# Performance work log

Measured on AMD Instinct MI355X. Metric: run time of the kernel, lower is better.

## Reference

```python
import jax, jax.numpy as jnp
import numpy as np

_DIR_INLIER = 0.9          # _HOUGHVOTING_DIRECTION_INLIER
_NUM_INLIER = 500          # _HOUGHVOTING_NUM_INLIER
_LABEL_THRESH = 500        # _LABEL2MASK_THRESHOL
NUM_CLASSES = 10
BS, H, W = 1, 240, 320


def setup_inputs() -> dict:
    key = jax.random.key(0)
    k_lab, k_cx, k_cy, k_nx, k_ny, k_nd = jax.random.split(key, 6)
    label = jax.random.randint(k_lab, (BS, H, W), 0, NUM_CLASSES + 1).astype(jnp.int32)
    xs = jnp.arange(W, dtype=jnp.float32)
    ys = jnp.arange(H, dtype=jnp.float32)
    xv, yv = jnp.meshgrid(xs, ys)  # [H, W] each
    # per-class ground-truth centers well inside the image so voting converges
    cxs = jax.random.uniform(k_cx, (NUM_CLASSES,), minval=40.0, maxval=W - 40.0)
    cys = jax.random.uniform(k_cy, (NUM_CLASSES,), minval=40.0, maxval=H - 40.0)
    dx = cxs[:, None, None] - xv[None]  # [C, H, W]
    dy = cys[:, None, None] - yv[None]
    nrm = jnp.sqrt(dx * dx + dy * dy) + 1e-6
    dirx = dx / nrm + 0.01 * jax.random.normal(k_nx, (NUM_CLASSES, H, W))
    diry = dy / nrm + 0.01 * jax.random.normal(k_ny, (NUM_CLASSES, H, W))
    depth = (1.0 + 0.3 * jnp.arange(NUM_CLASSES, dtype=jnp.float32))[:, None, None] \
        + 0.01 * jax.random.normal(k_nd, (NUM_CLASSES, H, W))
    cmap = jnp.stack([dirx, diry, depth], axis=1).reshape(3 * NUM_CLASSES, H, W)
    centermap = jnp.broadcast_to(cmap[None], (BS, 3 * NUM_CLASSES, H, W)).astype(jnp.float32)
    return {"label": label, "centermap": centermap}


def hough_voting(label, centermap, num_classes):
    bs, H_, W_ = label.shape
    xs = jnp.arange(W_, dtype=jnp.float32)
    ys = jnp.arange(H_, dtype=jnp.float32)
    xv, yv = jnp.meshgrid(xs, ys)            # [H, W]
    xsi = jnp.arange(W_, dtype=jnp.int32)
    all_centers, all_depths = [], []
    for b in range(bs):
        lab = label[b]
        row_c, row_d = [], []
        for cls in range(1, num_classes + 1):
            cmask = lab == cls                                    # [H, W]
            enough = cmask.sum() >= _LABEL_THRESH
            c3 = centermap[b, (cls - 1) * 3:(cls - 1) * 3 + 3]    # [3, H, W]
            slope = c3[1] / c3[0]                                  # dy/dx per pixel
            # every masked pixel votes along its line at every column x
            y_idx = jnp.round(yv[:, :, None] + slope[:, :, None] * (xs[None, None, :] - xv[:, :, None])).astype(jnp.int32)  # [H, W, W]
            valid = (y_idx >= 0) & (y_idx < H_) & cmask[:, :, None]
            bins = jnp.clip(y_idx, 0, H_ - 1) * W_ + xsi[None, None, :]
            hist = jnp.zeros(H_ * W_, jnp.float32).at[bins.ravel()].add(valid.ravel().astype(jnp.float32))
            cbin = jnp.argmax(hist)
            inlier_num = hist[cbin]
            cx = (cbin % W_).astype(jnp.float32)
            cy = (cbin // W_).astype(jnp.float32)
            # depth: mean of depth channel over direction-consistent class pixels
            disx = xv - cx
            disy = yv - cy
            dnrm = jnp.sqrt(disx * disx + disy * disy)
            dot = jnp.abs((disx / dnrm) * c3[0] + (disy / dnrm) * c3[1])  # nan at center -> compares False, as torch
            imask = (dot >= _DIR_INLIER) & cmask
            cnt = imask.sum().astype(jnp.float32)
            dsum = jnp.sum(jnp.where(imask, c3[2], 0.0))
            dmean = jnp.where(cnt > 0, dsum / jnp.maximum(cnt, 1.0), jnp.nan)
            trig = enough & (inlier_num > _NUM_INLIER)
            row_c.append(jnp.where(trig, jnp.stack([cx, cy]), jnp.zeros(2, jnp.float32)))
            row_d.append(jnp.where(trig, dmean, 0.0))
        all_centers.append(jnp.stack(row_c))
        all_depths.append(jnp.stack(row_d))
    return jnp.stack(all_centers), jnp.stack(all_depths)


def reference(label, centermap):
    return hough_voting(label, centermap, NUM_CLASSES)
```

## Files before the change

### kernel.cpp

```cpp
#include <hip/hip_runtime.h>
#include <stdint.h>

#define H 240
#define W 320
#define NPIX (H * W)
#define NCLS 10
#define COLS 4
#define VTHR 512
#define BIN_BITS 20
#define BIN_MASK 0xFFFFFu
#define POIS32 0xAAAAAAAAu


__global__ __launch_bounds__(256) void k_compact(const int* __restrict__ label,
                                                 const float* __restrict__ cm,
                                                 uint32_t* __restrict__ cls_cnt,
                                                 uint2* __restrict__ list) {
    __shared__ uint32_t lcnt[NCLS];
    __shared__ uint32_t lbase[NCLS];
    int p = blockIdx.x * 256 + threadIdx.x;
    if (threadIdx.x < NCLS) lcnt[threadIdx.x] = 0;
    __syncthreads();

    int l = label[p];
    bool match = (l >= 1 && l <= NCLS);
    int cls = l - 1;
    uint32_t li = 0;
    if (match) li = atomicAdd(&lcnt[cls], 1u);
    __syncthreads();

    if (threadIdx.x < NCLS) {
        uint32_t c = lcnt[threadIdx.x];
        lbase[threadIdx.x] = c ? (atomicAdd(&cls_cnt[threadIdx.x], c) - POIS32) : 0u;
    }
    __syncthreads();

    if (match) {
        float dirx = cm[(cls * 3 + 0) * NPIX + p];
        float diry = cm[(cls * 3 + 1) * NPIX + p];
        float slope = diry / dirx;
        int y = p / W, x = p - y * W;
        uint2 e;
        e.x = (uint32_t)(x | (y << 16));
        e.y = __float_as_uint(slope);
        list[cls * NPIX + lbase[cls] + li] = e;
    }
}

__global__ __launch_bounds__(VTHR) void k_vote(const uint32_t* __restrict__ cls_cnt,
                                               const uint2* __restrict__ list,
                                               unsigned long long* __restrict__ best) {
    int cls = blockIdx.y;
    int x0 = blockIdx.x * COLS;
    __shared__ uint32_t hist[COLS][H];
    __shared__ unsigned long long wred[VTHR / 64];
    for (int i = threadIdx.x; i < COLS * H; i += VTHR) ((uint32_t*)hist)[i] = 0;
    __syncthreads();

    int n = (int)(cls_cnt[cls] - POIS32);
    const uint2* lst = list + cls * NPIX;
    for (int i0 = 0; i0 < n; i0 += VTHR) {
        int i = i0 + (int)threadIdx.x;
        bool inb = (i < n);
        uint2 e;
        e.x = 0u; e.y = 0u;
        if (inb) e = lst[i];
        float slope = __uint_as_float(e.y);
        float xf = (float)(e.x & 0xFFFFu);
        float yf = (float)(e.x >> 16);
#pragma unroll
        for (int c = 0; c < COLS; ++c) {
            float dx = (float)(x0 + c) - xf;
            float r = rintf(yf + slope * dx);
            bool valid = inb && (r >= 0.0f) && (r <= (float)(H - 1));
            if (valid) atomicAdd(&hist[c][(int)r], 1u);
        }
    }
    __syncthreads();

    unsigned long long k = 0;
    for (int i = threadIdx.x; i < COLS * H; i += VTHR) {
        int c = i / H, y = i - c * H;
        uint32_t v = hist[c][y];
        uint32_t bin = (uint32_t)(y * W + x0 + c);
        unsigned long long key =
            ((unsigned long long)v << BIN_BITS) | (unsigned long long)(BIN_MASK - bin);
        if (key > k) k = key;
    }
#pragma unroll
    for (int off = 32; off > 0; off >>= 1) {
        unsigned long long o = __shfl_down(k, off);
        if (o > k) k = o;
    }
    if ((threadIdx.x & 63u) == 0u) wred[threadIdx.x >> 6] = k;
    __syncthreads();
    if (threadIdx.x == 0) {
        unsigned long long kk = wred[0];
#pragma unroll
        for (int w = 1; w < VTHR / 64; ++w) if (wred[w] > kk) kk = wred[w];
        atomicMax((long long*)&best[cls], (long long)kk);
    }
}

__global__ __launch_bounds__(256) void k_inlier_final(
    const int* __restrict__ label, const float* __restrict__ cm,
    const uint32_t* __restrict__ cls_cnt,
    const unsigned long long* __restrict__ best,
    uint32_t* __restrict__ icnt, float* __restrict__ dsum,
    uint32_t* __restrict__ done, float* __restrict__ out) {
    __shared__ float scx[NCLS], scy[NCLS];
    __shared__ uint32_t scnt[NCLS];
    __shared__ float ssum[NCLS];
    __shared__ int slast;
    int tid = threadIdx.x;
    if (tid < NCLS) {
        unsigned long long key = best[tid];
        uint32_t bin = BIN_MASK - (uint32_t)(key & BIN_MASK);
        scx[tid] = (float)(bin % W);
        scy[tid] = (float)(bin / W);
        scnt[tid] = 0u;
        ssum[tid] = 0.0f;
    }
    __syncthreads();

    int p = blockIdx.x * 256 + tid;
    int l = label[p];
    if (l >= 1 && l <= NCLS) {
        int cls = l - 1;
        int y = p / W, x = p - y * W;
        float disx = (float)x - scx[cls];
        float disy = (float)y - scy[cls];
        float dn = sqrtf(disx * disx + disy * disy);
        if (dn > 0.0f) {
            float c0 = cm[(cls * 3 + 0) * NPIX + p];
            float c1 = cm[(cls * 3 + 1) * NPIX + p];
            float dot = fabsf((disx / dn) * c0 + (disy / dn) * c1);
            if (dot >= 0.9f) {
                atomicAdd(&scnt[cls], 1u);
                atomicAdd(&ssum[cls], cm[(cls * 3 + 2) * NPIX + p]);
            }
        }
    }
    __syncthreads();

    if (tid < NCLS) {
        if (scnt[tid]) atomicAdd(&icnt[tid], scnt[tid]);
        if (ssum[tid] != 0.0f) atomicAdd(&dsum[tid], ssum[tid]);
    }
    if (tid == 0) {
        __threadfence();
        uint32_t d = atomicAdd(done, 1u);
        slast = (d == POIS32 + (uint32_t)(gridDim.x - 1)) ? 1 : 0;
    }
    __syncthreads();

    if (slast && tid < NCLS) {
        uint32_t tc = atomicAdd(&icnt[tid], 0u) - POIS32;
        float td = atomicAdd(&dsum[tid], 0.0f);
        unsigned long long key = best[tid];
        uint32_t hv = (uint32_t)(key >> BIN_BITS);
        bool trig = ((cls_cnt[tid] - POIS32) >= 500u) && (hv > 500u);
        float c = (float)tc;
        float dm = (c > 0.0f) ? (td / fmaxf(c, 1.0f)) : __builtin_nanf("");
        out[tid * 2 + 0] = trig ? scx[tid] : 0.0f;
        out[tid * 2 + 1] = trig ? scy[tid] : 0.0f;
        out[2 * NCLS + tid] = trig ? dm : 0.0f;
    }
}

extern "C" void kernel_launch(void* const* d_in, const int* in_sizes, int n_in,
                              void* d_out, int out_size, void* d_ws, size_t ws_size,
                              hipStream_t stream) {
    const int* label = (const int*)d_in[0];
    const float* cm = (const float*)d_in[1];
    float* out = (float*)d_out;
    char* ws = (char*)d_ws;

    uint32_t* cls_cnt = (uint32_t*)(ws + 0);
    unsigned long long* best = (unsigned long long*)(ws + 64);
    uint32_t* icnt = (uint32_t*)(ws + 192);
    float* dsum = (float*)(ws + 256);
    uint32_t* done = (uint32_t*)(ws + 320);
    uint2* list = (uint2*)(ws + 512);

    k_compact<<<NPIX / 256, 256, 0, stream>>>(label, cm, cls_cnt, list);
    k_vote<<<dim3(W / COLS, NCLS), VTHR, 0, stream>>>(cls_cnt, list, best);
    k_inlier_final<<<NPIX / 256, 256, 0, stream>>>(label, cm, cls_cnt, best,
                                                   icnt, dsum, done, out);
}
```

Measured before the change: 98.35 us.

## Fuse inlier/depth pass into vote kernel via last-block-per-class epilogue

Removes the separate inlier/final kernel. The last vote block to finish for each class, detected with a per-class atomic done counter, reads the best bin and iterates the compacted class pixel list to count direction inliers and sum depth, then writes that class's outputs. This drops a kernel launch and a full-image label scan. In exchange the inlier work for each class is serialized into one block at the tail of voting, with gathered centermap reads.

```diff
diff --git a/kernel.cpp b/kernel.cpp
--- a/kernel.cpp
+++ b/kernel.cpp
@@ -49,18 +49,26 @@
 
 __global__ __launch_bounds__(VTHR) void k_vote(const uint32_t* __restrict__ cls_cnt,
                                                const uint2* __restrict__ list,
-                                               unsigned long long* __restrict__ best) {
+                                               const float* __restrict__ cm,
+                                               unsigned long long* __restrict__ best,
+                                               uint32_t* __restrict__ done_cls,
+                                               float* __restrict__ out) {
     int cls = blockIdx.y;
     int x0 = blockIdx.x * COLS;
     __shared__ uint32_t hist[COLS][H];
     __shared__ unsigned long long wred[VTHR / 64];
-    for (int i = threadIdx.x; i < COLS * H; i += VTHR) ((uint32_t*)hist)[i] = 0;
+    __shared__ int slastS;
+    __shared__ float scx, scy;
+    __shared__ uint32_t shv, scnt;
+    __shared__ float ssum;
+    int tid = threadIdx.x;
+    for (int i = tid; i < COLS * H; i += VTHR) ((uint32_t*)hist)[i] = 0;
     __syncthreads();
 
     int n = (int)(cls_cnt[cls] - POIS32);
     const uint2* lst = list + cls * NPIX;
     for (int i0 = 0; i0 < n; i0 += VTHR) {
-        int i = i0 + (int)threadIdx.x;
+        int i = i0 + tid;
         bool inb = (i < n);
         uint2 e;
         e.x = 0u; e.y = 0u;
@@ -79,7 +87,7 @@
     __syncthreads();
 
     unsigned long long k = 0;
-    for (int i = threadIdx.x; i < COLS * H; i += VTHR) {
+    for (int i = tid; i < COLS * H; i += VTHR) {
         int c = i / H, y = i - c * H;
         uint32_t v = hist[c][y];
         uint32_t bin = (uint32_t)(y * W + x0 + c);
@@ -92,79 +100,58 @@
         unsigned long long o = __shfl_down(k, off);
         if (o > k) k = o;
     }
-    if ((threadIdx.x & 63u) == 0u) wred[threadIdx.x >> 6] = k;
+    if ((tid & 63) == 0) wred[tid >> 6] = k;
     __syncthreads();
-    if (threadIdx.x == 0) {
+    if (tid == 0) {
         unsigned long long kk = wred[0];
 #pragma unroll
         for (int w = 1; w < VTHR / 64; ++w) if (wred[w] > kk) kk = wred[w];
         atomicMax((long long*)&best[cls], (long long)kk);
+        __threadfence();
+        uint32_t d = atomicAdd(&done_cls[cls], 1u);
+        slastS = (d == POIS32 + (uint32_t)(gridDim.x - 1)) ? 1 : 0;
     }
-}
+    __syncthreads();
+    if (!slastS) return;
 
-__global__ __launch_bounds__(256) void k_inlier_final(
-    const int* __restrict__ label, const float* __restrict__ cm,
-    const uint32_t* __restrict__ cls_cnt,
-    const unsigned long long* __restrict__ best,
-    uint32_t* __restrict__ icnt, float* __restrict__ dsum,
-    uint32_t* __restrict__ done, float* __restrict__ out) {
-    __shared__ float scx[NCLS], scy[NCLS];
-    __shared__ uint32_t scnt[NCLS];
-    __shared__ float ssum[NCLS];
-    __shared__ int slast;
-    int tid = threadIdx.x;
-    if (tid < NCLS) {
-        unsigned long long key = best[tid];
+    if (tid == 0) {
+        unsigned long long key = atomicAdd(&best[cls], 0ull);
         uint32_t bin = BIN_MASK - (uint32_t)(key & BIN_MASK);
-        scx[tid] = (float)(bin % W);
-        scy[tid] = (float)(bin / W);
-        scnt[tid] = 0u;
-        ssum[tid] = 0.0f;
+        scx = (float)(bin % W);
+        scy = (float)(bin / W);
+        shv = (uint32_t)(key >> BIN_BITS);
+        scnt = 0u;
+        ssum = 0.0f;
     }
     __syncthreads();
 
-    int p = blockIdx.x * 256 + tid;
-    int l = label[p];
-    if (l >= 1 && l <= NCLS) {
-        int cls = l - 1;
-        int y = p / W, x = p - y * W;
-        float disx = (float)x - scx[cls];
-        float disy = (float)y - scy[cls];
+    const float* cm0 = cm + (cls * 3 + 0) * NPIX;
+    const float* cm1 = cm + (cls * 3 + 1) * NPIX;
+    const float* cm2 = cm + (cls * 3 + 2) * NPIX;
+    for (int i = tid; i < n; i += VTHR) {
+        uint2 e = lst[i];
+        int x = (int)(e.x & 0xFFFFu), y = (int)(e.x >> 16);
+        int p = y * W + x;
+        float disx = (float)x - scx;
+        float disy = (float)y - scy;
         float dn = sqrtf(disx * disx + disy * disy);
         if (dn > 0.0f) {
-            float c0 = cm[(cls * 3 + 0) * NPIX + p];
-            float c1 = cm[(cls * 3 + 1) * NPIX + p];
-            float dot = fabsf((disx / dn) * c0 + (disy / dn) * c1);
+            float dot = fabsf((disx / dn) * cm0[p] + (disy / dn) * cm1[p]);
             if (dot >= 0.9f) {
-                atomicAdd(&scnt[cls], 1u);
-                atomicAdd(&ssum[cls], cm[(cls * 3 + 2) * NPIX + p]);
+                atomicAdd(&scnt, 1u);
+                atomicAdd(&ssum, cm2[p]);
             }
         }
     }
     __syncthreads();
 
-    if (tid < NCLS) {
-        if (scnt[tid]) atomicAdd(&icnt[tid], scnt[tid]);
-        if (ssum[tid] != 0.0f) atomicAdd(&dsum[tid], ssum[tid]);
-    }
     if (tid == 0) {
-        __threadfence();
-        uint32_t d = atomicAdd(done, 1u);
-        slast = (d == POIS32 + (uint32_t)(gridDim.x - 1)) ? 1 : 0;
-    }
-    __syncthreads();
-
-    if (slast && tid < NCLS) {
-        uint32_t tc = atomicAdd(&icnt[tid], 0u) - POIS32;
-        float td = atomicAdd(&dsum[tid], 0.0f);
-        unsigned long long key = best[tid];
-        uint32_t hv = (uint32_t)(key >> BIN_BITS);
-        bool trig = ((cls_cnt[tid] - POIS32) >= 500u) && (hv > 500u);
-        float c = (float)tc;
-        float dm = (c > 0.0f) ? (td / fmaxf(c, 1.0f)) : __builtin_nanf("");
-        out[tid * 2 + 0] = trig ? scx[tid] : 0.0f;
-        out[tid * 2 + 1] = trig ? scy[tid] : 0.0f;
-        out[2 * NCLS + tid] = trig ? dm : 0.0f;
+        bool trig = ((uint32_t)n >= 500u) && (shv > 500u);
+        float c = (float)scnt;
+        float dm = (c > 0.0f) ? (ssum / fmaxf(c, 1.0f)) : __builtin_nanf("");
+        out[cls * 2 + 0] = trig ? scx : 0.0f;
+        out[cls * 2 + 1] = trig ? scy : 0.0f;
+        out[2 * NCLS + cls] = trig ? dm : 0.0f;
     }
 }
 
@@ -178,13 +165,10 @@
 
     uint32_t* cls_cnt = (uint32_t*)(ws + 0);
     unsigned long long* best = (unsigned long long*)(ws + 64);
-    uint32_t* icnt = (uint32_t*)(ws + 192);
-    float* dsum = (float*)(ws + 256);
-    uint32_t* done = (uint32_t*)(ws + 320);
+    uint32_t* done_cls = (uint32_t*)(ws + 320);
     uint2* list = (uint2*)(ws + 512);
 
     k_compact<<<NPIX / 256, 256, 0, stream>>>(label, cm, cls_cnt, list);
-    k_vote<<<dim3(W / COLS, NCLS), VTHR, 0, stream>>>(cls_cnt, list, best);
-    k_inlier_final<<<NPIX / 256, 256, 0, stream>>>(label, cm, cls_cnt, best,
-                                                   icnt, dsum, done, out);
+    k_vote<<<dim3(W / COLS, NCLS), VTHR, 0, stream>>>(cls_cnt, list, cm, best,
+                                                      done_cls, out);
 }
```

After: 146.0 us. +48.4%, slower.

## Fuse vote and inlier kernels with spin-wait and prefetch inlier loads

Applied to the files above, without the earlier changes.

Merges the voting and inlier/final kernels into one launch. Inlier blocks sit after the vote blocks in the grid: they load label and centermap values first, then spin on a global counter until every vote block has finished. The voting loop also software-prefetches the next list entry. This removes one kernel launch and hides the inlier loads behind voting, but relies on vote blocks being scheduled before the spinning inlier blocks, which risks deadlock or wasted occupancy.

```diff
diff --git a/kernel.cpp b/kernel.cpp
--- a/kernel.cpp
+++ b/kernel.cpp
@@ -7,6 +7,8 @@
 #define NCLS 10
 #define COLS 4
 #define VTHR 512
+#define VOTE_BLKS ((W / COLS) * NCLS)
+#define INL_BLKS (NPIX / VTHR)
 #define BIN_BITS 20
 #define BIN_MASK 0xFFFFFu
 #define POIS32 0xAAAAAAAAu
@@ -47,74 +49,97 @@
     }
 }
 
-__global__ __launch_bounds__(VTHR) void k_vote(const uint32_t* __restrict__ cls_cnt,
-                                               const uint2* __restrict__ list,
-                                               unsigned long long* __restrict__ best) {
-    int cls = blockIdx.y;
-    int x0 = blockIdx.x * COLS;
+__global__ __launch_bounds__(VTHR) void k_vote_inlier(
+    const int* __restrict__ label, const float* __restrict__ cm,
+    const uint32_t* __restrict__ cls_cnt, const uint2* __restrict__ list,
+    unsigned long long* __restrict__ best,
+    uint32_t* __restrict__ icnt, float* __restrict__ dsum,
+    uint32_t* __restrict__ vdone, uint32_t* __restrict__ idone,
+    float* __restrict__ out) {
     __shared__ uint32_t hist[COLS][H];
     __shared__ unsigned long long wred[VTHR / 64];
-    for (int i = threadIdx.x; i < COLS * H; i += VTHR) ((uint32_t*)hist)[i] = 0;
-    __syncthreads();
-
-    int n = (int)(cls_cnt[cls] - POIS32);
-    const uint2* lst = list + cls * NPIX;
-    for (int i0 = 0; i0 < n; i0 += VTHR) {
-        int i = i0 + (int)threadIdx.x;
-        bool inb = (i < n);
-        uint2 e;
-        e.x = 0u; e.y = 0u;
-        if (inb) e = lst[i];
-        float slope = __uint_as_float(e.y);
-        float xf = (float)(e.x & 0xFFFFu);
-        float yf = (float)(e.x >> 16);
-#pragma unroll
-        for (int c = 0; c < COLS; ++c) {
-            float dx = (float)(x0 + c) - xf;
-            float r = rintf(yf + slope * dx);
-            bool valid = inb && (r >= 0.0f) && (r <= (float)(H - 1));
-            if (valid) atomicAdd(&hist[c][(int)r], 1u);
-        }
-    }
-    __syncthreads();
-
-    unsigned long long k = 0;
-    for (int i = threadIdx.x; i < COLS * H; i += VTHR) {
-        int c = i / H, y = i - c * H;
-        uint32_t v = hist[c][y];
-        uint32_t bin = (uint32_t)(y * W + x0 + c);
-        unsigned long long key =
-            ((unsigned long long)v << BIN_BITS) | (unsigned long long)(BIN_MASK - bin);
-        if (key > k) k = key;
-    }
-#pragma unroll
-    for (int off = 32; off > 0; off >>= 1) {
-        unsigned long long o = __shfl_down(k, off);
-        if (o > k) k = o;
-    }
-    if ((threadIdx.x & 63u) == 0u) wred[threadIdx.x >> 6] = k;
-    __syncthreads();
-    if (threadIdx.x == 0) {
-        unsigned long long kk = wred[0];
-#pragma unroll
-        for (int w = 1; w < VTHR / 64; ++w) if (wred[w] > kk) kk = wred[w];
-        atomicMax((long long*)&best[cls], (long long)kk);
-    }
-}
-
-__global__ __launch_bounds__(256) void k_inlier_final(
-    const int* __restrict__ label, const float* __restrict__ cm,
-    const uint32_t* __restrict__ cls_cnt,
-    const unsigned long long* __restrict__ best,
-    uint32_t* __restrict__ icnt, float* __restrict__ dsum,
-    uint32_t* __restrict__ done, float* __restrict__ out) {
     __shared__ float scx[NCLS], scy[NCLS];
     __shared__ uint32_t scnt[NCLS];
     __shared__ float ssum[NCLS];
     __shared__ int slast;
-    int tid = threadIdx.x;
+    int tid = (int)threadIdx.x;
+    int bid = (int)blockIdx.x;
+
+    if (bid < VOTE_BLKS) {
+        int cls = bid / (W / COLS);
+        int x0 = (bid % (W / COLS)) * COLS;
+        for (int i = tid; i < COLS * H; i += VTHR) ((uint32_t*)hist)[i] = 0;
+        __syncthreads();
+
+        int n = (int)(cls_cnt[cls] - POIS32);
+        const uint2* lst = list + cls * NPIX;
+        uint2 e;
+        e.x = 0u; e.y = 0u;
+        if (tid < n) e = lst[tid];
+        for (int i0 = 0; i0 < n; i0 += VTHR) {
+            bool inb = (i0 + tid < n);
+            uint2 cur = e;
+            e.x = 0u; e.y = 0u;
+            int inext = i0 + VTHR + tid;
+            if (inext < n) e = lst[inext];
+            float slope = __uint_as_float(cur.y);
+            float xf = (float)(cur.x & 0xFFFFu);
+            float yf = (float)(cur.x >> 16);
+#pragma unroll
+            for (int c = 0; c < COLS; ++c) {
+                float dx = (float)(x0 + c) - xf;
+                float r = rintf(yf + slope * dx);
+                bool valid = inb && (r >= 0.0f) && (r <= (float)(H - 1));
+                if (valid) atomicAdd(&hist[c][(int)r], 1u);
+            }
+        }
+        __syncthreads();
+
+        unsigned long long k = 0;
+        for (int i = tid; i < COLS * H; i += VTHR) {
+            int c = i / H, y = i - c * H;
+            uint32_t v = hist[c][y];
+            uint32_t bin = (uint32_t)(y * W + x0 + c);
+            unsigned long long key =
+                ((unsigned long long)v << BIN_BITS) | (unsigned long long)(BIN_MASK - bin);
+            if (key > k) k = key;
+        }
+#pragma unroll
+        for (int off = 32; off > 0; off >>= 1) {
+            unsigned long long o = __shfl_down(k, off);
+            if (o > k) k = o;
+        }
+        if ((tid & 63) == 0) wred[tid >> 6] = k;
+        __syncthreads();
+        if (tid == 0) {
+            unsigned long long kk = wred[0];
+#pragma unroll
+            for (int w = 1; w < VTHR / 64; ++w) if (wred[w] > kk) kk = wred[w];
+            atomicMax((long long*)&best[cls], (long long)kk);
+            __threadfence();
+            atomicAdd(vdone, 1u);
+        }
+        return;
+    }
+
+    int p = (bid - VOTE_BLKS) * VTHR + tid;
+    int l = label[p];
+    bool match = (l >= 1 && l <= NCLS);
+    int cls = match ? l - 1 : 0;
+    float c0 = cm[(cls * 3 + 0) * NPIX + p];
+    float c1 = cm[(cls * 3 + 1) * NPIX + p];
+    float c2 = cm[(cls * 3 + 2) * NPIX + p];
+    int y = p / W, x = p - y * W;
+
+    if (tid == 0) {
+        while ((uint32_t)(atomicAdd(vdone, 0u) - POIS32) < (uint32_t)VOTE_BLKS)
+            __builtin_amdgcn_s_sleep(8);
+    }
+    __syncthreads();
+    __threadfence();
+
     if (tid < NCLS) {
-        unsigned long long key = best[tid];
+        unsigned long long key = atomicAdd(&best[tid], 0ull);
         uint32_t bin = BIN_MASK - (uint32_t)(key & BIN_MASK);
         scx[tid] = (float)(bin % W);
         scy[tid] = (float)(bin / W);
@@ -123,21 +148,15 @@
     }
     __syncthreads();
 
-    int p = blockIdx.x * 256 + tid;
-    int l = label[p];
-    if (l >= 1 && l <= NCLS) {
-        int cls = l - 1;
-        int y = p / W, x = p - y * W;
+    if (match) {
         float disx = (float)x - scx[cls];
         float disy = (float)y - scy[cls];
         float dn = sqrtf(disx * disx + disy * disy);
         if (dn > 0.0f) {
-            float c0 = cm[(cls * 3 + 0) * NPIX + p];
-            float c1 = cm[(cls * 3 + 1) * NPIX + p];
             float dot = fabsf((disx / dn) * c0 + (disy / dn) * c1);
             if (dot >= 0.9f) {
                 atomicAdd(&scnt[cls], 1u);
-                atomicAdd(&ssum[cls], cm[(cls * 3 + 2) * NPIX + p]);
+                atomicAdd(&ssum[cls], c2);
             }
         }
     }
@@ -149,15 +168,15 @@
     }
     if (tid == 0) {
         __threadfence();
-        uint32_t d = atomicAdd(done, 1u);
-        slast = (d == POIS32 + (uint32_t)(gridDim.x - 1)) ? 1 : 0;
+        uint32_t d = atomicAdd(idone, 1u);
+        slast = (d == POIS32 + (uint32_t)(INL_BLKS - 1)) ? 1 : 0;
     }
     __syncthreads();
 
     if (slast && tid < NCLS) {
         uint32_t tc = atomicAdd(&icnt[tid], 0u) - POIS32;
         float td = atomicAdd(&dsum[tid], 0.0f);
-        unsigned long long key = best[tid];
+        unsigned long long key = atomicAdd(&best[tid], 0ull);
         uint32_t hv = (uint32_t)(key >> BIN_BITS);
         bool trig = ((cls_cnt[tid] - POIS32) >= 500u) && (hv > 500u);
         float c = (float)tc;
@@ -180,11 +199,11 @@
     unsigned long long* best = (unsigned long long*)(ws + 64);
     uint32_t* icnt = (uint32_t*)(ws + 192);
     float* dsum = (float*)(ws + 256);
-    uint32_t* done = (uint32_t*)(ws + 320);
+    uint32_t* vdone = (uint32_t*)(ws + 320);
+    uint32_t* idone = (uint32_t*)(ws + 324);
     uint2* list = (uint2*)(ws + 512);
 
     k_compact<<<NPIX / 256, 256, 0, stream>>>(label, cm, cls_cnt, list);
-    k_vote<<<dim3(W / COLS, NCLS), VTHR, 0, stream>>>(cls_cnt, list, best);
-    k_inlier_final<<<NPIX / 256, 256, 0, stream>>>(label, cm, cls_cnt, best,
-                                                   icnt, dsum, done, out);
+    k_vote_inlier<<<VOTE_BLKS + INL_BLKS, VTHR, 0, stream>>>(
+        label, cm, cls_cnt, list, best, icnt, dsum, vdone, idone, out);
 }
```

Result: slower. 156.0 us (+58.7%).
